# Optimization experiments

Measured on AMD Instinct MI355X. Metric: run time of the kernel, lower is better.

The kernel has to match this reference:

```python
import jax, jax.numpy as jnp
import numpy as np


def setup_inputs() -> dict:
    key = jax.random.key(0)
    kx, kq, kk, kv = jax.random.split(key, 4)
    B, C, H, W = 4, 256, 64, 64
    scale = 1.0 / np.sqrt(C)
    return {
        "x": jax.random.normal(kx, (B, C, H, W), dtype=jnp.float32),
        "Wq": jax.random.normal(kq, (C, C), dtype=jnp.float32) * scale,
        "Wk": jax.random.normal(kk, (C, C), dtype=jnp.float32) * scale,
        "Wv": jax.random.normal(kv, (C, C), dtype=jnp.float32) * scale,
        "gamma": jnp.ones((1,), dtype=jnp.float32) * 0.1,
    }


def reference(x, Wq, Wk, Wv, gamma):
    B, C, H, W = x.shape
    N = H * W
    xt = x.reshape(B, C, N)  # tokens along last axis
    # 1x1 convs == channel matmuls: (O,C) x (B,C,N) -> (B,O,N)
    q = jnp.einsum('oc,bcn->bon', Wq, xt)
    k = jnp.einsum('oc,bcn->bon', Wk, xt)
    v = jnp.einsum('oc,bcn->bon', Wv, xt)
    # energy[b,n,m] = sum_o q[b,o,n] * k[b,o,m]  (q^T k)
    energy = jnp.einsum('bon,bom->bnm', q, k)
    attn = jax.nn.softmax(energy, axis=-1)  # softmax over m (keys)
    # out[b,c,n] = sum_m v[b,c,m] * attn[b,n,m]  (v @ attn^T)
    out = jnp.einsum('bcm,bnm->bcn', v, attn).reshape(B, C, H, W)
    return gamma * out + x
```

## Files before the change

### kernel.cpp

```cpp
#include <hip/hip_runtime.h>
#include <stdint.h>

#define B_ 4
#define C_ 256
#define N_ 4096
#define TK 32

using floatx4 = __attribute__((ext_vector_type(4))) float;
using halfx8  = __attribute__((ext_vector_type(8))) _Float16;

__device__ __forceinline__ float bf16_to_f(uint16_t u) {
    union { uint32_t u; float f; } c; c.u = ((uint32_t)u) << 16; return c.f;
}
__device__ __forceinline__ uint16_t f_to_bf16(float f) {
    union { float f; uint32_t u; } c; c.f = f;
    uint32_t u = c.u;
    u += 0x7FFFu + ((u >> 16) & 1u);
    return (uint16_t)(u >> 16);
}

__device__ __forceinline__ void async_copy16(const void* g, void* l) {
    __builtin_amdgcn_global_load_lds(
        (const __attribute__((address_space(1))) void*)g,
        (__attribute__((address_space(3))) void*)l, 16, 0, 0);
}

__global__ void sniff_kernel(const uint16_t* __restrict__ wq_u16, int* __restrict__ flag) {
    __shared__ int cnt;
    if (threadIdx.x == 0) cnt = 0;
    __syncthreads();
    int local = 0;
    for (int i = threadIdx.x; i < 8192; i += 256) {
        int e = (wq_u16[i] >> 7) & 0xFF;
        if (e >= 132) local++;
    }
    atomicAdd(&cnt, local);
    __syncthreads();
    if (threadIdx.x == 0) *flag = (cnt > 64) ? 1 : 0;
}

__global__ void wconv_kernel(const void* __restrict__ wq,
                             const void* __restrict__ wk,
                             const void* __restrict__ wv,
                             _Float16* __restrict__ wf,
                             const int* __restrict__ flag) {
    const int isf32 = *flag;
    int idx = blockIdx.x * 256 + threadIdx.x;
    int mat = idx >> 16;
    int off = idx & 65535;
    const void* src = (mat == 0) ? wq : ((mat == 1) ? wk : wv);
    float v = isf32 ? ((const float*)src)[off] : bf16_to_f(((const uint16_t*)src)[off]);
    wf[idx] = (_Float16)v;
}

__global__ __launch_bounds__(256) void proj_kernel(
    const void* __restrict__ x_raw,
    const _Float16* __restrict__ wf,
    _Float16* __restrict__ qt,
    _Float16* __restrict__ kt,
    _Float16* __restrict__ v,
    const int* __restrict__ flag) {
    const int isf32 = *flag;
    const int b = blockIdx.y;
    const int mat = blockIdx.z;
    const int n0 = blockIdx.x * 64;
    const int tid = threadIdx.x;
    const int w = tid >> 6;
    const int L = tid & 63;
    const int lane15 = L & 15;
    const int quad = L >> 4;
    const int n = n0 + w * 16 + lane15;

    halfx8 bfrag[8];
    const size_t xbase = (size_t)b * C_ * N_;
    if (isf32) {
        const float* xb = (const float*)x_raw + xbase;
#pragma unroll
        for (int cs = 0; cs < 8; ++cs) {
            const int cbase = cs * 32 + quad * 8;
            halfx8 f;
#pragma unroll
            for (int j = 0; j < 8; ++j)
                f[j] = (_Float16)xb[(size_t)(cbase + j) * N_ + n];
            bfrag[cs] = f;
        }
    } else {
        const uint16_t* xb = (const uint16_t*)x_raw + xbase;
#pragma unroll
        for (int cs = 0; cs < 8; ++cs) {
            const int cbase = cs * 32 + quad * 8;
            halfx8 f;
#pragma unroll
            for (int j = 0; j < 8; ++j)
                f[j] = (_Float16)bf16_to_f(xb[(size_t)(cbase + j) * N_ + n]);
            bfrag[cs] = f;
        }
    }

    const _Float16* wm = wf + mat * (C_ * C_);
#pragma unroll 4
    for (int ot = 0; ot < 16; ++ot) {
        const int obase = ot * 16;
        floatx4 acc = {0.f, 0.f, 0.f, 0.f};
        const _Float16* wrow = wm + (size_t)(obase + lane15) * C_ + quad * 8;
#pragma unroll
        for (int cs = 0; cs < 8; ++cs) {
            halfx8 af = *(const halfx8*)(wrow + cs * 32);
            acc = __builtin_amdgcn_mfma_f32_16x16x32_f16(af, bfrag[cs], acc, 0, 0, 0);
        }
        if (mat < 2) {
            _Float16* dst = (mat == 0 ? qt : kt) +
                            ((size_t)b * N_ + n) * C_ + obase + quad * 4;
            union { _Float16 h[4]; unsigned long long u64; } pk;
#pragma unroll
            for (int r = 0; r < 4; ++r) pk.h[r] = (_Float16)acc[r];
            *(unsigned long long*)dst = pk.u64;
        } else {
            _Float16* dst = v + ((size_t)b * C_ + obase + quad * 4) * N_ + n;
#pragma unroll
            for (int r = 0; r < 4; ++r) dst[(size_t)r * N_] = (_Float16)acc[r];
        }
    }
}

__global__ __launch_bounds__(1024) void attn_kernel(
    const _Float16* __restrict__ qt,
    const _Float16* __restrict__ kt,
    const _Float16* __restrict__ v,
    _Float16* __restrict__ O_part,
    float* __restrict__ m_part,
    float* __restrict__ l_part) {
    const int l = blockIdx.x;
    const int combo = (l & 7) | ((l >> 7) << 3);
    const int qt_i = (l >> 3) & 15;
    const int b = combo >> 2;
    const int ks = combo & 3;
    const int q0 = qt_i * 256;
    const int tid = threadIdx.x;
    const int w = tid >> 6;
    const int L = tid & 63;
    const int lane15 = L & 15;
    const int quad = L >> 4;

    __shared__ _Float16 Kb0[32][256], Kb1[32][256];
    __shared__ _Float16 Vb0[256][32], Vb1[256][32];
    extern __shared__ _Float16 Ps_dyn[];

    _Float16* PsW = Ps_dyn + w * 512;

    const int rowK = 2 * w + (L >> 5);
    const int kSrcCol = (((L & 31) ^ (rowK & 7)) << 3);
    const int cV = 16 * w + (L >> 2);
    const int vSrcCol = (((L & 3) ^ ((cV >> 1) & 3)) << 3);

    const _Float16* ktb = kt + (size_t)b * N_ * C_;
    const _Float16* vb  = v  + (size_t)b * C_ * N_;
    const _Float16* kSrc = ktb + (size_t)rowK * C_ + kSrcCol;
    const _Float16* vSrc = vb + (size_t)cV * N_ + vSrcCol;

    halfx8 qfrag[8];
    {
        const _Float16* qrow = qt + ((size_t)b * N_ + q0 + w * 16 + lane15) * C_ + quad * 8;
#pragma unroll
        for (int cs = 0; cs < 8; ++cs)
            qfrag[cs] = __builtin_nontemporal_load((const halfx8*)(qrow + cs * 32));
    }

    floatx4 o_acc[16];
#pragma unroll
    for (int i = 0; i < 16; ++i) o_acc[i] = (floatx4){0.f, 0.f, 0.f, 0.f};
    float m_r = -1e30f, l_r = 0.f;

    const int kbeg = ks * 1024;
    const int swK = lane15 & 7;
    const int swV = (lane15 >> 1) & 3;

    async_copy16(kSrc + (size_t)kbeg * C_, (char*)&Kb0[0][0] + w * 1024);
    async_copy16(vSrc + kbeg,              (char*)&Vb0[0][0] + w * 1024);
    __syncthreads();

    int cur = 0;
    for (int it = 0; it < 32; ++it) {
        if (it < 31) {
            const int kn = kbeg + (it + 1) * TK;
            char* kd = (char*)(cur ? &Kb0[0][0] : &Kb1[0][0]) + w * 1024;
            char* vd = (char*)(cur ? &Vb0[0][0] : &Vb1[0][0]) + w * 1024;
            async_copy16(kSrc + (size_t)kn * C_, kd);
            async_copy16(vSrc + kn, vd);
        }
        const _Float16* Kc = cur ? &Kb1[0][0] : &Kb0[0][0];
        const _Float16* Vc = cur ? &Vb1[0][0] : &Vb0[0][0];

        floatx4 s_acc[2];
        s_acc[0] = (floatx4){0.f, 0.f, 0.f, 0.f};
        s_acc[1] = (floatx4){0.f, 0.f, 0.f, 0.f};
#pragma unroll
        for (int t = 0; t < 2; ++t) {
            const _Float16* kr = Kc + (t * 16 + lane15) * 256;
#pragma unroll
            for (int cs = 0; cs < 8; ++cs) {
                const int pch = (quad + 4 * cs) ^ swK;
                halfx8 kf = *(const halfx8*)(kr + pch * 8);
                s_acc[t] = __builtin_amdgcn_mfma_f32_16x16x32_f16(kf, qfrag[cs], s_acc[t], 0, 0, 0);
            }
        }

        float rmax = fmaxf(fmaxf(fmaxf(s_acc[0][0], s_acc[0][1]), fmaxf(s_acc[0][2], s_acc[0][3])),
                           fmaxf(fmaxf(s_acc[1][0], s_acc[1][1]), fmaxf(s_acc[1][2], s_acc[1][3])));
        rmax = fmaxf(rmax, __shfl_xor(rmax, 16));
        rmax = fmaxf(rmax, __shfl_xor(rmax, 32));
        float mn = fmaxf(m_r, rmax);
        float alpha = __expf(m_r - mn);
        m_r = mn;
        float p0[4], p1[4];
        float psum = 0.f;
#pragma unroll
        for (int r = 0; r < 4; ++r) {
            p0[r] = __expf(s_acc[0][r] - mn);
            p1[r] = __expf(s_acc[1][r] - mn);
            psum += p0[r] + p1[r];
        }
        psum += __shfl_xor(psum, 16);
        psum += __shfl_xor(psum, 32);
        l_r = l_r * alpha + psum;

        union { _Float16 h[4]; unsigned long long u64; } pk0, pk1;
#pragma unroll
        for (int r = 0; r < 4; ++r) { pk0.h[r] = (_Float16)p0[r]; pk1.h[r] = (_Float16)p1[r]; }
        *(unsigned long long*)(PsW + lane15 * 32 + quad * 4)      = pk0.u64;
        *(unsigned long long*)(PsW + lane15 * 32 + 16 + quad * 4) = pk1.u64;

#pragma unroll
        for (int i = 0; i < 16; ++i) o_acc[i] *= alpha;
        halfx8 pfrag = *(const halfx8*)(PsW + lane15 * 32 + quad * 8);
#pragma unroll
        for (int ct = 0; ct < 16; ++ct) {
            const int c = ct * 16 + lane15;
            halfx8 vf = *(const halfx8*)(Vc + c * 32 + ((quad ^ swV) * 8));
            o_acc[ct] = __builtin_amdgcn_mfma_f32_16x16x32_f16(vf, pfrag, o_acc[ct], 0, 0, 0);
        }

        __syncthreads();
        cur ^= 1;
    }

    const size_t pbase = (size_t)((b * 16 + qt_i) * 4 + ks);
    _Float16* ob = O_part + (pbase * 256 + (size_t)(w * 16 + lane15)) * 256;
#pragma unroll
    for (int ct = 0; ct < 16; ++ct) {
        union { _Float16 h[4]; unsigned long long u64; } pk;
#pragma unroll
        for (int r = 0; r < 4; ++r) pk.h[r] = (_Float16)o_acc[ct][r];
        __builtin_nontemporal_store(pk.u64, (unsigned long long*)(ob + ct * 16 + quad * 4));
    }
    if (quad == 0) {
        m_part[pbase * 256 + w * 16 + lane15] = m_r;
        l_part[pbase * 256 + w * 16 + lane15] = l_r;
    }
}

__global__ __launch_bounds__(256) void reduce_kernel(
    const void* __restrict__ x_raw,
    const _Float16* __restrict__ O_part,
    const float* __restrict__ m_part,
    const float* __restrict__ l_part,
    const void* __restrict__ gamma_p,
    void* __restrict__ out,
    const int* __restrict__ flag) {
    const int isf32 = *flag;
    const int b = blockIdx.y;
    const int tid = threadIdx.x;
    const int q = tid & 63;
    const int wv = tid >> 6;
    const int n = blockIdx.x * 64 + q;
    const int qt_i = n >> 8;
    const int qq = n & 255;

    const size_t sbase = (size_t)(b * 16 + qt_i) * 4;
    float m0 = m_part[(sbase + 0) * 256 + qq], m1 = m_part[(sbase + 1) * 256 + qq],
          m2 = m_part[(sbase + 2) * 256 + qq], m3 = m_part[(sbase + 3) * 256 + qq];
    float l0 = l_part[(sbase + 0) * 256 + qq], l1 = l_part[(sbase + 1) * 256 + qq],
          l2 = l_part[(sbase + 2) * 256 + qq], l3 = l_part[(sbase + 3) * 256 + qq];
    float M = fmaxf(fmaxf(m0, m1), fmaxf(m2, m3));
    float w0 = __expf(m0 - M), w1 = __expf(m1 - M), w2 = __expf(m2 - M), w3 = __expf(m3 - M);
    float denom = w0 * l0 + w1 * l1 + w2 * l2 + w3 * l3;
    float g = isf32 ? ((const float*)gamma_p)[0] : bf16_to_f(((const uint16_t*)gamma_p)[0]);
    float s = g / denom;

    const _Float16* o0 = O_part + sbase * 65536 + (size_t)qq * 256;
#pragma unroll
    for (int ch = 0; ch < 8; ++ch) {
        const int c0 = wv * 64 + ch * 8;
        halfx8 a     = __builtin_nontemporal_load((const halfx8*)(o0 + c0));
        halfx8 bpart = __builtin_nontemporal_load((const halfx8*)(o0 + 65536 + c0));
        halfx8 cpart = __builtin_nontemporal_load((const halfx8*)(o0 + 131072 + c0));
        halfx8 dpart = __builtin_nontemporal_load((const halfx8*)(o0 + 196608 + c0));
#pragma unroll
        for (int j = 0; j < 8; ++j) {
            float acc = w0 * (float)a[j] + w1 * (float)bpart[j]
                      + w2 * (float)cpart[j] + w3 * (float)dpart[j];
            size_t off = ((size_t)b * 256 + c0 + j) * 4096 + n;
            float xv = isf32 ? __builtin_nontemporal_load((const float*)x_raw + off)
                             : bf16_to_f(((const uint16_t*)x_raw)[off]);
            float val = s * acc + xv;
            if (isf32) __builtin_nontemporal_store(val, (float*)out + off);
            else ((uint16_t*)out)[off] = f_to_bf16(val);
        }
    }
}

__global__ __launch_bounds__(256, 2) void attn_full_kernel(
    const void* __restrict__ x_raw,
    const _Float16* __restrict__ qt,
    const _Float16* __restrict__ kt,
    const _Float16* __restrict__ v,
    const void* __restrict__ gamma_p,
    void* __restrict__ out,
    const int* __restrict__ flag) {
    const int isf32 = *flag;
    const int b = blockIdx.y;
    const int q0 = blockIdx.x * 64;
    const int tid = threadIdx.x;
    const int w = tid >> 6;
    const int L = tid & 63;
    const int lane15 = L & 15;
    const int quad = L >> 4;

    __shared__ _Float16 Kt_s[TK][260];
    __shared__ _Float16 Vs[C_][36];
    __shared__ _Float16 Ps[4][16][36];
    __shared__ float alpha_s[4][16];
    __shared__ float l_s[4][16];

    halfx8 qfrag[8];
    {
        const _Float16* qrow = qt + ((size_t)b * N_ + q0 + w * 16 + lane15) * C_ + quad * 8;
#pragma unroll
        for (int cs = 0; cs < 8; ++cs) qfrag[cs] = *(const halfx8*)(qrow + cs * 32);
    }
    floatx4 o_acc[16];
#pragma unroll
    for (int i = 0; i < 16; ++i) o_acc[i] = (floatx4){0.f, 0.f, 0.f, 0.f};
    float m_r[4], l_r[4];
#pragma unroll
    for (int r = 0; r < 4; ++r) { m_r[r] = -1e30f; l_r[r] = 0.f; }
    const _Float16* ktb = kt + (size_t)b * N_ * C_;
    const _Float16* vb  = v  + (size_t)b * C_ * N_;

    for (int k0 = 0; k0 < N_; k0 += TK) {
#pragma unroll
        for (int p = 0; p < 4; ++p) {
            int idx = p * 256 + tid;
            int key = idx >> 5, ch = idx & 31;
            *(halfx8*)(&Kt_s[key][ch * 8]) =
                *(const halfx8*)(ktb + (size_t)(k0 + key) * C_ + ch * 8);
        }
#pragma unroll
        for (int p = 0; p < 4; ++p) {
            int idx = p * 256 + tid;
            int c = idx >> 2, ch = idx & 3;
            *(halfx8*)(&Vs[c][ch * 8]) =
                *(const halfx8*)(vb + (size_t)c * N_ + k0 + ch * 8);
        }
        __syncthreads();
        floatx4 s_acc[2];
        s_acc[0] = (floatx4){0.f, 0.f, 0.f, 0.f};
        s_acc[1] = (floatx4){0.f, 0.f, 0.f, 0.f};
#pragma unroll
        for (int ktile = 0; ktile < 2; ++ktile) {
            const _Float16* krow = &Kt_s[ktile * 16 + lane15][quad * 8];
#pragma unroll
            for (int cs = 0; cs < 8; ++cs) {
                halfx8 bf = *(const halfx8*)(krow + cs * 32);
                s_acc[ktile] = __builtin_amdgcn_mfma_f32_16x16x32_f16(qfrag[cs], bf, s_acc[ktile], 0, 0, 0);
            }
        }
        float rmax[4], psum[4], p0[4], p1[4], alpha[4];
#pragma unroll
        for (int r = 0; r < 4; ++r) rmax[r] = fmaxf(s_acc[0][r], s_acc[1][r]);
#pragma unroll
        for (int mask = 1; mask <= 8; mask <<= 1)
#pragma unroll
            for (int r = 0; r < 4; ++r) rmax[r] = fmaxf(rmax[r], __shfl_xor(rmax[r], mask));
#pragma unroll
        for (int r = 0; r < 4; ++r) {
            float mn = fmaxf(m_r[r], rmax[r]);
            alpha[r] = __expf(m_r[r] - mn);
            m_r[r] = mn;
            p0[r] = __expf(s_acc[0][r] - mn);
            p1[r] = __expf(s_acc[1][r] - mn);
            psum[r] = p0[r] + p1[r];
        }
#pragma unroll
        for (int mask = 1; mask <= 8; mask <<= 1)
#pragma unroll
            for (int r = 0; r < 4; ++r) psum[r] += __shfl_xor(psum[r], mask);
#pragma unroll
        for (int r = 0; r < 4; ++r) l_r[r] = l_r[r] * alpha[r] + psum[r];
#pragma unroll
        for (int r = 0; r < 4; ++r) {
            Ps[w][quad * 4 + r][lane15]      = (_Float16)p0[r];
            Ps[w][quad * 4 + r][16 + lane15] = (_Float16)p1[r];
        }
        if (lane15 == 0) {
#pragma unroll
            for (int r = 0; r < 4; ++r) alpha_s[w][quad * 4 + r] = alpha[r];
        }
        __syncthreads();
        float av = alpha_s[w][lane15];
#pragma unroll
        for (int i = 0; i < 16; ++i) {
            o_acc[i][0] *= av; o_acc[i][1] *= av; o_acc[i][2] *= av; o_acc[i][3] *= av;
        }
        halfx8 pfrag = *(const halfx8*)(&Ps[w][lane15][quad * 8]);
#pragma unroll
        for (int ct = 0; ct < 16; ++ct) {
            halfx8 vf = *(const halfx8*)(&Vs[ct * 16 + lane15][quad * 8]);
            o_acc[ct] = __builtin_amdgcn_mfma_f32_16x16x32_f16(vf, pfrag, o_acc[ct], 0, 0, 0);
        }
        __syncthreads();
    }
    if (lane15 == 0) {
#pragma unroll
        for (int r = 0; r < 4; ++r) l_s[w][quad * 4 + r] = l_r[r];
    }
    __syncthreads();
    float linv = 1.0f / l_s[w][lane15];
    float g = isf32 ? ((const float*)gamma_p)[0] : bf16_to_f(((const uint16_t*)gamma_p)[0]);
    const int n_out = q0 + w * 16 + lane15;
#pragma unroll
    for (int ct = 0; ct < 16; ++ct)
#pragma unroll
        for (int r = 0; r < 4; ++r) {
            int c = ct * 16 + quad * 4 + r;
            size_t off = ((size_t)b * C_ + c) * N_ + n_out;
            float val = g * o_acc[ct][r] * linv +
                        (isf32 ? ((const float*)x_raw)[off] : bf16_to_f(((const uint16_t*)x_raw)[off]));
            if (isf32) ((float*)out)[off] = val;
            else ((uint16_t*)out)[off] = f_to_bf16(val);
        }
}

extern "C" void kernel_launch(void* const* d_in, const int* in_sizes, int n_in,
                              void* d_out, int out_size, void* d_ws, size_t ws_size,
                              hipStream_t stream) {
    const void* x  = d_in[0];
    const void* wq = d_in[1];
    const void* wk = d_in[2];
    const void* wv = d_in[3];
    const void* gm = d_in[4];

    char* ws = (char*)d_ws;
    int* flag    = (int*)ws;
    _Float16* wf = (_Float16*)(ws + 4096);
    size_t o0 = 4096 + 393216;
    _Float16* qt = (_Float16*)(ws + o0);
    _Float16* kt = (_Float16*)(ws + o0 + 8388608);
    _Float16* v  = (_Float16*)(ws + o0 + 2 * 8388608);
    size_t o1 = o0 + 3 * 8388608;
    _Float16* opart = (_Float16*)(ws + o1);
    float* mpart = (float*)(ws + o1 + 33554432);
    float* lpart = (float*)(ws + o1 + 33554432 + 262144);
    const size_t need = o1 + 33554432 + 2 * 262144;

    sniff_kernel<<<dim3(1), dim3(256), 0, stream>>>((const uint16_t*)wq, flag);
    wconv_kernel<<<dim3(768), dim3(256), 0, stream>>>(wq, wk, wv, wf, flag);
    proj_kernel<<<dim3(64, 4, 3), dim3(256), 0, stream>>>(x, wf, qt, kt, v, flag);
    if (ws_size >= need) {
        attn_kernel<<<dim3(256), dim3(1024), 16384, stream>>>(qt, kt, v, opart, mpart, lpart);
        reduce_kernel<<<dim3(64, 4), dim3(256), 0, stream>>>(x, opart, mpart, lpart, gm, d_out, flag);
    } else {
        attn_full_kernel<<<dim3(64, 4), dim3(256), 0, stream>>>(x, qt, kt, v, gm, d_out, flag);
    }
}
```

Baseline: 290.7 us.

## Process two query tiles per wave in attention kernel with 512 threads

```diff
diff --git a/kernel.cpp b/kernel.cpp
--- a/kernel.cpp
+++ b/kernel.cpp
@@ -123,7 +123,7 @@
     }
 }
 
-__global__ __launch_bounds__(1024) void attn_kernel(
+__global__ __launch_bounds__(512, 2) void attn_kernel(
     const _Float16* __restrict__ qt,
     const _Float16* __restrict__ kt,
     const _Float16* __restrict__ v,
@@ -146,54 +146,66 @@
     __shared__ _Float16 Vb0[256][32], Vb1[256][32];
     extern __shared__ _Float16 Ps_dyn[];
 
-    _Float16* PsW = Ps_dyn + w * 512;
+    _Float16* PsW = Ps_dyn + w * 1280;
 
     const int rowK = 2 * w + (L >> 5);
-    const int kSrcCol = (((L & 31) ^ (rowK & 7)) << 3);
-    const int cV = 16 * w + (L >> 2);
-    const int vSrcCol = (((L & 3) ^ ((cV >> 1) & 3)) << 3);
+    const int kCol = (((L & 31) ^ (rowK & 7)) << 3);
+    const int cV   = 16 * w + (L >> 2);
+    const int vCol = (((L & 3) ^ ((L >> 3) & 3)) << 3);
 
     const _Float16* ktb = kt + (size_t)b * N_ * C_;
     const _Float16* vb  = v  + (size_t)b * C_ * N_;
-    const _Float16* kSrc = ktb + (size_t)rowK * C_ + kSrcCol;
-    const _Float16* vSrc = vb + (size_t)cV * N_ + vSrcCol;
-
-    halfx8 qfrag[8];
-    {
-        const _Float16* qrow = qt + ((size_t)b * N_ + q0 + w * 16 + lane15) * C_ + quad * 8;
+    const _Float16* kSrc0 = ktb + (size_t)rowK * C_ + kCol;
+    const _Float16* kSrc1 = ktb + (size_t)(rowK + 16) * C_ + kCol;
+    const _Float16* vSrc0 = vb + (size_t)cV * N_ + vCol;
+    const _Float16* vSrc1 = vb + (size_t)(cV + 128) * N_ + vCol;
+    const int ldsOff = w * 1024;
+
+    halfx8 qfrag[2][8];
+#pragma unroll
+    for (int j = 0; j < 2; ++j) {
+        const _Float16* qrow = qt + ((size_t)b * N_ + q0 + w * 32 + j * 16 + lane15) * C_ + quad * 8;
 #pragma unroll
         for (int cs = 0; cs < 8; ++cs)
-            qfrag[cs] = __builtin_nontemporal_load((const halfx8*)(qrow + cs * 32));
-    }
-
-    floatx4 o_acc[16];
-#pragma unroll
-    for (int i = 0; i < 16; ++i) o_acc[i] = (floatx4){0.f, 0.f, 0.f, 0.f};
-    float m_r = -1e30f, l_r = 0.f;
+            qfrag[j][cs] = __builtin_nontemporal_load((const halfx8*)(qrow + cs * 32));
+    }
+
+    floatx4 o_acc[2][16];
+#pragma unroll
+    for (int j = 0; j < 2; ++j)
+#pragma unroll
+        for (int i = 0; i < 16; ++i) o_acc[j][i] = (floatx4){0.f, 0.f, 0.f, 0.f};
+    float m_r[2] = {-1e30f, -1e30f}, l_r[2] = {0.f, 0.f};
 
     const int kbeg = ks * 1024;
     const int swK = lane15 & 7;
     const int swV = (lane15 >> 1) & 3;
 
-    async_copy16(kSrc + (size_t)kbeg * C_, (char*)&Kb0[0][0] + w * 1024);
-    async_copy16(vSrc + kbeg,              (char*)&Vb0[0][0] + w * 1024);
+    async_copy16(kSrc0 + (size_t)kbeg * C_, (char*)&Kb0[0][0] + ldsOff);
+    async_copy16(kSrc1 + (size_t)kbeg * C_, (char*)&Kb0[0][0] + 8192 + ldsOff);
+    async_copy16(vSrc0 + kbeg,              (char*)&Vb0[0][0] + ldsOff);
+    async_copy16(vSrc1 + kbeg,              (char*)&Vb0[0][0] + 8192 + ldsOff);
     __syncthreads();
 
     int cur = 0;
     for (int it = 0; it < 32; ++it) {
         if (it < 31) {
             const int kn = kbeg + (it + 1) * TK;
-            char* kd = (char*)(cur ? &Kb0[0][0] : &Kb1[0][0]) + w * 1024;
-            char* vd = (char*)(cur ? &Vb0[0][0] : &Vb1[0][0]) + w * 1024;
-            async_copy16(kSrc + (size_t)kn * C_, kd);
-            async_copy16(vSrc + kn, vd);
+            char* kd = (char*)(cur ? &Kb0[0][0] : &Kb1[0][0]);
+            char* vd = (char*)(cur ? &Vb0[0][0] : &Vb1[0][0]);
+            async_copy16(kSrc0 + (size_t)kn * C_, kd + ldsOff);
+            async_copy16(kSrc1 + (size_t)kn * C_, kd + 8192 + ldsOff);
+            async_copy16(vSrc0 + kn, vd + ldsOff);
+            async_copy16(vSrc1 + kn, vd + 8192 + ldsOff);
         }
         const _Float16* Kc = cur ? &Kb1[0][0] : &Kb0[0][0];
         const _Float16* Vc = cur ? &Vb1[0][0] : &Vb0[0][0];
 
-        floatx4 s_acc[2];
-        s_acc[0] = (floatx4){0.f, 0.f, 0.f, 0.f};
-        s_acc[1] = (floatx4){0.f, 0.f, 0.f, 0.f};
+        floatx4 s_acc[2][2];
+#pragma unroll
+        for (int j = 0; j < 2; ++j)
+#pragma unroll
+            for (int t = 0; t < 2; ++t) s_acc[j][t] = (floatx4){0.f, 0.f, 0.f, 0.f};
 #pragma unroll
         for (int t = 0; t < 2; ++t) {
             const _Float16* kr = Kc + (t * 16 + lane15) * 256;
@@ -201,43 +213,54 @@
             for (int cs = 0; cs < 8; ++cs) {
                 const int pch = (quad + 4 * cs) ^ swK;
                 halfx8 kf = *(const halfx8*)(kr + pch * 8);
-                s_acc[t] = __builtin_amdgcn_mfma_f32_16x16x32_f16(kf, qfrag[cs], s_acc[t], 0, 0, 0);
+                s_acc[0][t] = __builtin_amdgcn_mfma_f32_16x16x32_f16(kf, qfrag[0][cs], s_acc[0][t], 0, 0, 0);
+                s_acc[1][t] = __builtin_amdgcn_mfma_f32_16x16x32_f16(kf, qfrag[1][cs], s_acc[1][t], 0, 0, 0);
             }
         }
 
-        float rmax = fmaxf(fmaxf(fmaxf(s_acc[0][0], s_acc[0][1]), fmaxf(s_acc[0][2], s_acc[0][3])),
-                           fmaxf(fmaxf(s_acc[1][0], s_acc[1][1]), fmaxf(s_acc[1][2], s_acc[1][3])));
-        rmax = fmaxf(rmax, __shfl_xor(rmax, 16));
-        rmax = fmaxf(rmax, __shfl_xor(rmax, 32));
-        float mn = fmaxf(m_r, rmax);
-        float alpha = __expf(m_r - mn);
-        m_r = mn;
-        float p0[4], p1[4];
-        float psum = 0.f;
-#pragma unroll
-        for (int r = 0; r < 4; ++r) {
-            p0[r] = __expf(s_acc[0][r] - mn);
-            p1[r] = __expf(s_acc[1][r] - mn);
-            psum += p0[r] + p1[r];
-        }
-        psum += __shfl_xor(psum, 16);
-        psum += __shfl_xor(psum, 32);
-        l_r = l_r * alpha + psum;
-
-        union { _Float16 h[4]; unsigned long long u64; } pk0, pk1;
-#pragma unroll
-        for (int r = 0; r < 4; ++r) { pk0.h[r] = (_Float16)p0[r]; pk1.h[r] = (_Float16)p1[r]; }
-        *(unsigned long long*)(PsW + lane15 * 32 + quad * 4)      = pk0.u64;
-        *(unsigned long long*)(PsW + lane15 * 32 + 16 + quad * 4) = pk1.u64;
-
-#pragma unroll
-        for (int i = 0; i < 16; ++i) o_acc[i] *= alpha;
-        halfx8 pfrag = *(const halfx8*)(PsW + lane15 * 32 + quad * 8);
+        float alpha[2];
+#pragma unroll
+        for (int j = 0; j < 2; ++j) {
+            float rmax = fmaxf(
+                fmaxf(fmaxf(s_acc[j][0][0], s_acc[j][0][1]), fmaxf(s_acc[j][0][2], s_acc[j][0][3])),
+                fmaxf(fmaxf(s_acc[j][1][0], s_acc[j][1][1]), fmaxf(s_acc[j][1][2], s_acc[j][1][3])));
+            rmax = fmaxf(rmax, __shfl_xor(rmax, 16));
+            rmax = fmaxf(rmax, __shfl_xor(rmax, 32));
+            float mn = fmaxf(m_r[j], rmax);
+            alpha[j] = __expf(m_r[j] - mn);
+            m_r[j] = mn;
+            float p0[4], p1[4];
+            float psum = 0.f;
+#pragma unroll
+            for (int r = 0; r < 4; ++r) {
+                p0[r] = __expf(s_acc[j][0][r] - mn);
+                p1[r] = __expf(s_acc[j][1][r] - mn);
+                psum += p0[r] + p1[r];
+            }
+            psum += __shfl_xor(psum, 16);
+            psum += __shfl_xor(psum, 32);
+            l_r[j] = l_r[j] * alpha[j] + psum;
+
+            union { _Float16 h[4]; unsigned long long u64; } pk0, pk1;
+#pragma unroll
+            for (int r = 0; r < 4; ++r) { pk0.h[r] = (_Float16)p0[r]; pk1.h[r] = (_Float16)p1[r]; }
+            _Float16* prow = PsW + (j * 16 + lane15) * 40;
+            *(unsigned long long*)(prow + quad * 4)      = pk0.u64;
+            *(unsigned long long*)(prow + 16 + quad * 4) = pk1.u64;
+        }
+
+#pragma unroll
+        for (int j = 0; j < 2; ++j)
+#pragma unroll
+            for (int i = 0; i < 16; ++i) o_acc[j][i] *= alpha[j];
+        halfx8 pfrag0 = *(const halfx8*)(PsW + lane15 * 40 + quad * 8);
+        halfx8 pfrag1 = *(const halfx8*)(PsW + (16 + lane15) * 40 + quad * 8);
 #pragma unroll
         for (int ct = 0; ct < 16; ++ct) {
             const int c = ct * 16 + lane15;
             halfx8 vf = *(const halfx8*)(Vc + c * 32 + ((quad ^ swV) * 8));
-            o_acc[ct] = __builtin_amdgcn_mfma_f32_16x16x32_f16(vf, pfrag, o_acc[ct], 0, 0, 0);
+            o_acc[0][ct] = __builtin_amdgcn_mfma_f32_16x16x32_f16(vf, pfrag0, o_acc[0][ct], 0, 0, 0);
+            o_acc[1][ct] = __builtin_amdgcn_mfma_f32_16x16x32_f16(vf, pfrag1, o_acc[1][ct], 0, 0, 0);
         }
 
         __syncthreads();
@@ -245,17 +268,20 @@
     }
 
     const size_t pbase = (size_t)((b * 16 + qt_i) * 4 + ks);
-    _Float16* ob = O_part + (pbase * 256 + (size_t)(w * 16 + lane15)) * 256;
-#pragma unroll
-    for (int ct = 0; ct < 16; ++ct) {
-        union { _Float16 h[4]; unsigned long long u64; } pk;
-#pragma unroll
-        for (int r = 0; r < 4; ++r) pk.h[r] = (_Float16)o_acc[ct][r];
-        __builtin_nontemporal_store(pk.u64, (unsigned long long*)(ob + ct * 16 + quad * 4));
-    }
-    if (quad == 0) {
-        m_part[pbase * 256 + w * 16 + lane15] = m_r;
-        l_part[pbase * 256 + w * 16 + lane15] = l_r;
+#pragma unroll
+    for (int j = 0; j < 2; ++j) {
+        _Float16* ob = O_part + (pbase * 256 + (size_t)(w * 32 + j * 16 + lane15)) * 256;
+#pragma unroll
+        for (int ct = 0; ct < 16; ++ct) {
+            union { _Float16 h[4]; unsigned long long u64; } pk;
+#pragma unroll
+            for (int r = 0; r < 4; ++r) pk.h[r] = (_Float16)o_acc[j][ct][r];
+            __builtin_nontemporal_store(pk.u64, (unsigned long long*)(ob + ct * 16 + quad * 4));
+        }
+        if (quad == 0) {
+            m_part[pbase * 256 + w * 32 + j * 16 + lane15] = m_r[j];
+            l_part[pbase * 256 + w * 32 + j * 16 + lane15] = l_r[j];
+        }
     }
 }
 
@@ -467,7 +493,7 @@
     wconv_kernel<<<dim3(768), dim3(256), 0, stream>>>(wq, wk, wv, wf, flag);
     proj_kernel<<<dim3(64, 4, 3), dim3(256), 0, stream>>>(x, wf, qt, kt, v, flag);
     if (ws_size >= need) {
-        attn_kernel<<<dim3(256), dim3(1024), 16384, stream>>>(qt, kt, v, opart, mpart, lpart);
+        attn_kernel<<<dim3(256), dim3(512), 20480, stream>>>(qt, kt, v, opart, mpart, lpart);
         reduce_kernel<<<dim3(64, 4), dim3(256), 0, stream>>>(x, opart, mpart, lpart, gm, d_out, flag);
     } else {
         attn_full_kernel<<<dim3(64, 4), dim3(256), 0, stream>>>(x, qt, kt, v, gm, d_out, flag);
```

Measured after the change: 265.3 us. -8.7%, faster.
